# Kernel tuning notes

Hardware: AMD Instinct MI355X
Metric: run time of the kernel (lower is better)

## Reference

```python
import jax, jax.numpy as jnp
import numpy as np

N_NODES = 50000
N_EDGES = 1600000
IN_DIM = 256
HID = 128
HEADS = 1
N_CLASSES = 40
NEG_SLOPE = 0.2


def gat_conv(x, W, a_src, a_dst, b, src, dst, concat):
    """PyG GATConv (eval mode). x: [N, F_in]; W: [H*C, F_in]; a_*: [H, C]; b: bias."""
    N = x.shape[0]
    H, C = a_src.shape
    h = (x @ W.T).reshape(N, H, C)                       # [N, H, C]
    alpha_src = jnp.sum(h * a_src, axis=-1)              # [N, H]
    alpha_dst = jnp.sum(h * a_dst, axis=-1)              # [N, H]
    e = jax.nn.leaky_relu(alpha_src[src] + alpha_dst[dst], NEG_SLOPE)  # [E, H]
    # scatter-softmax over incoming edges of each destination node
    m = jax.ops.segment_max(e, dst, num_segments=N)
    m = jnp.where(jnp.isfinite(m), m, 0.0)               # nodes with no in-edges
    ex = jnp.exp(e - m[dst])
    denom = jax.ops.segment_sum(ex, dst, num_segments=N)
    alpha = ex / jnp.maximum(denom[dst], 1e-16)          # [E, H]
    out = jax.ops.segment_sum(h[src] * alpha[..., None], dst, num_segments=N)  # [N, H, C]
    out = out.reshape(N, H * C) if concat else out.mean(axis=1)
    return out + b


def setup_inputs() -> dict:
    key = jax.random.key(0)
    ks = jax.random.split(key, 10)
    glorot = lambda k, shape: jax.random.normal(k, shape, jnp.float32) * np.sqrt(2.0 / (shape[0] + shape[-1]))
    x = jax.random.normal(ks[0], (N_NODES, IN_DIM), jnp.float32)
    edge_index = jax.random.randint(ks[1], (2, N_EDGES), 0, N_NODES, jnp.int64)
    # layer 0: in=IN_DIM -> hidden, heads=HEADS, concat=True
    W0 = glorot(ks[2], (HEADS * HID, IN_DIM))
    a_src0 = glorot(ks[3], (HEADS, HID))
    a_dst0 = glorot(ks[4], (HEADS, HID))
    b0 = jnp.zeros((HEADS * HID,), jnp.float32)
    # layer 1: in=hidden*heads -> n_classes, concat=False
    W1 = glorot(ks[5], (HEADS * N_CLASSES, HEADS * HID))
    a_src1 = glorot(ks[6], (HEADS, N_CLASSES))
    a_dst1 = glorot(ks[7], (HEADS, N_CLASSES))
    b1 = jnp.zeros((N_CLASSES,), jnp.float32)
    return {"x": x, "edge_index": edge_index,
            "W0": W0, "a_src0": a_src0, "a_dst0": a_dst0, "b0": b0,
            "W1": W1, "a_src1": a_src1, "a_dst1": a_dst1, "b1": b1}


def reference(x, edge_index, W0, a_src0, a_dst0, b0, W1, a_src1, a_dst1, b1):
    N = x.shape[0]
    # PyG GATConv default add_self_loops=True (each layer adds them transiently)
    loop = jnp.arange(N, dtype=edge_index.dtype)
    src = jnp.concatenate([edge_index[0], loop])
    dst = jnp.concatenate([edge_index[1], loop])
    h = gat_conv(x, W0, a_src0, a_dst0, b0, src, dst, concat=True)
    h = jax.nn.relu(h)  # dropout is identity in eval mode
    out = gat_conv(h, W1, a_src1, a_dst1, b1, src, dst, concat=False)
    return out
```

## Files before the change

kernel.cpp:

```cpp
#include <hip/hip_runtime.h>
#include <hip/hip_bf16.h>

#define N_NODES 50000
#define N_EDGES 1600000
#define ET (N_EDGES + N_NODES)
#define IN_DIM 256
#define HID 128
#define NCLS 40
#define NEG 0.2f
#define NBUCK 391
#define CHUNK 4096

typedef short bf16x8 __attribute__((ext_vector_type(8)));
typedef float f32x4  __attribute__((ext_vector_type(4)));

__device__ __forceinline__ unsigned pk2(float a, float b) {
    __hip_bfloat16 ha = __float2bfloat16(a), hb = __float2bfloat16(b);
    unsigned short ua = *(unsigned short*)&ha, ub = *(unsigned short*)&hb;
    return (unsigned)ua | ((unsigned)ub << 16);
}
__device__ __forceinline__ float blo(unsigned u) { return __uint_as_float(u << 16); }
__device__ __forceinline__ float bhi(unsigned u) { return __uint_as_float(u & 0xffff0000u); }

__global__ __launch_bounds__(256) void k_bin_count(const int* __restrict__ ei,
                                                   int* __restrict__ bcnt) {
    __shared__ int hist[NBUCK];
    int t = threadIdx.x;
    for (int i = t; i < NBUCK; i += 256) hist[i] = 0;
    __syncthreads();
    int base = blockIdx.x * CHUNK;
    #pragma unroll
    for (int j = 0; j < 16; ++j) {
        int i = base + j * 256 + t;
        if (i < ET) {
            int d = (i < N_EDGES) ? ei[N_EDGES + i] : (i - N_EDGES);
            atomicAdd(&hist[d >> 7], 1);
        }
    }
    __syncthreads();
    for (int i = t; i < NBUCK; i += 256) if (hist[i]) atomicAdd(&bcnt[i], hist[i]);
}

__global__ __launch_bounds__(512) void k_bin_scan(const int* __restrict__ bcnt,
                                                  int* __restrict__ cstart,
                                                  int* __restrict__ cursor,
                                                  int* __restrict__ rp) {
    __shared__ int s[512];
    int t = threadIdx.x;
    int v = (t < NBUCK) ? bcnt[t] : 0;
    s[t] = v;
    __syncthreads();
    for (int off = 1; off < 512; off <<= 1) {
        int u = (t >= off) ? s[t - off] : 0;
        __syncthreads();
        s[t] += u;
        __syncthreads();
    }
    int ex = s[t] - v;
    if (t < NBUCK) { cstart[t] = ex; cursor[t] = ex; }
    if (t == 0) { cstart[NBUCK] = ET; rp[N_NODES] = ET; }
}

__global__ __launch_bounds__(256) void k_bin_scatter(const int* __restrict__ ei,
                                                     int* __restrict__ cursor,
                                                     unsigned int* __restrict__ buf) {
    __shared__ int sd[CHUNK];
    __shared__ int hist[NBUCK];
    __shared__ int wbase[NBUCK];
    int t = threadIdx.x;
    for (int i = t; i < NBUCK; i += 256) hist[i] = 0;
    __syncthreads();
    int base = blockIdx.x * CHUNK;
    #pragma unroll
    for (int j = 0; j < 16; ++j) {
        int i = base + j * 256 + t;
        int d = -1;
        if (i < ET) d = (i < N_EDGES) ? ei[N_EDGES + i] : (i - N_EDGES);
        sd[j * 256 + t] = d;
        if (d >= 0) atomicAdd(&hist[d >> 7], 1);
    }
    __syncthreads();
    for (int i = t; i < NBUCK; i += 256) {
        int h = hist[i];
        wbase[i] = h ? atomicAdd(&cursor[i], h) : 0;
        hist[i] = 0;
    }
    __syncthreads();
    #pragma unroll
    for (int j = 0; j < 16; ++j) {
        int i = base + j * 256 + t;
        int d = sd[j * 256 + t];
        if (d >= 0) {
            int s_ = (i < N_EDGES) ? ei[i] : d;
            int b = d >> 7;
            int off = atomicAdd(&hist[b], 1);
            buf[wbase[b] + off] = ((unsigned)(d & 127) << 16) | (unsigned)s_;
        }
    }
}

__global__ __launch_bounds__(256) void k_bucket_build(const unsigned int* __restrict__ buf,
                                                      const int* __restrict__ cstart,
                                                      int* __restrict__ rp,
                                                      int* __restrict__ csr) {
    __shared__ int cnt[128], rpl[128], cur[128];
    int b = blockIdx.x;
    int t = threadIdx.x;
    int lo = cstart[b], hi = cstart[b + 1];
    if (t < 128) cnt[t] = 0;
    __syncthreads();
    for (int i = lo + t; i < hi; i += 256) atomicAdd(&cnt[buf[i] >> 16], 1);
    __syncthreads();
    if (t == 0) {
        int run = 0;
        #pragma unroll
        for (int l = 0; l < 128; ++l) { rpl[l] = run; run += cnt[l]; }
    }
    __syncthreads();
    if (t < 128) {
        int node = b * 128 + t;
        if (node < N_NODES) rp[node] = lo + rpl[t];
        cur[t] = 0;
    }
    __syncthreads();
    for (int i = lo + t; i < hi; i += 256) {
        unsigned v = buf[i];
        int dl = v >> 16;
        int off = atomicAdd(&cur[dl], 1);
        csr[lo + rpl[dl] + off] = (int)(v & 0xffffu);
    }
}

__global__ __launch_bounds__(256) void k_gemm0(
    const float* __restrict__ x, const float* __restrict__ W0,
    const float* __restrict__ a_s, const float* __restrict__ a_d,
    unsigned short* __restrict__ h0b, float* __restrict__ as0, float* __restrict__ ad0) {
    __shared__ unsigned sA[64 * 36];
    __shared__ unsigned sB[128 * 36];
    int t = threadIdx.x;
    int n0 = blockIdx.x * 64;
    int w = t >> 6, lane = t & 63;
    int rw = lane & 15, q = lane >> 4;
    f32x4 acc[8];
    #pragma unroll
    for (int n = 0; n < 8; ++n) acc[n] = (f32x4){0.f, 0.f, 0.f, 0.f};

    for (int kc = 0; kc < IN_DIM; kc += 64) {
        #pragma unroll
        for (int i = 0; i < 4; ++i) {
            int f = i * 256 + t;
            int r = f >> 4, fq = f & 15;
            float4 v = make_float4(0.f, 0.f, 0.f, 0.f);
            if (n0 + r < N_NODES)
                v = *(const float4*)&x[(size_t)(n0 + r) * IN_DIM + kc + fq * 4];
            *(uint2*)&sA[r * 36 + fq * 2] = make_uint2(pk2(v.x, v.y), pk2(v.z, v.w));
        }
        #pragma unroll
        for (int i = 0; i < 8; ++i) {
            int f = i * 256 + t;
            int c = f >> 4, fq = f & 15;
            float4 v = *(const float4*)&W0[(size_t)c * IN_DIM + kc + fq * 4];
            *(uint2*)&sB[c * 36 + fq * 2] = make_uint2(pk2(v.x, v.y), pk2(v.z, v.w));
        }
        __syncthreads();
        #pragma unroll
        for (int ks = 0; ks < 2; ++ks) {
            bf16x8 af = *(const bf16x8*)((const unsigned short*)sA + (16 * w + rw) * 72 + ks * 32 + q * 8);
            #pragma unroll
            for (int n = 0; n < 8; ++n) {
                bf16x8 bfr = *(const bf16x8*)((const unsigned short*)sB + (n * 16 + rw) * 72 + ks * 32 + q * 8);
                acc[n] = __builtin_amdgcn_mfma_f32_16x16x32_bf16(af, bfr, acc[n], 0, 0, 0);
            }
        }
        __syncthreads();
    }

    float asv[8], adv[8];
    #pragma unroll
    for (int n = 0; n < 8; ++n) { asv[n] = a_s[n * 16 + rw]; adv[n] = a_d[n * 16 + rw]; }
    float ps[4] = {0.f, 0.f, 0.f, 0.f}, pd[4] = {0.f, 0.f, 0.f, 0.f};
    #pragma unroll
    for (int n = 0; n < 8; ++n)
        #pragma unroll
        for (int reg = 0; reg < 4; ++reg) {
            float vv = acc[n][reg];
            ps[reg] += vv * asv[n];
            pd[reg] += vv * adv[n];
        }
    #pragma unroll
    for (int reg = 0; reg < 4; ++reg) {
        int node = n0 + 16 * w + q * 4 + reg;
        if (node < N_NODES) {
            #pragma unroll
            for (int n = 0; n < 8; ++n) {
                __hip_bfloat16 hb = __float2bfloat16(acc[n][reg]);
                h0b[(size_t)node * HID + n * 16 + rw] = *(unsigned short*)&hb;
            }
        }
    }
    #pragma unroll
    for (int reg = 0; reg < 4; ++reg)
        #pragma unroll
        for (int off = 1; off < 16; off <<= 1) {
            ps[reg] += __shfl_xor(ps[reg], off);
            pd[reg] += __shfl_xor(pd[reg], off);
        }
    if (rw == 0) {
        #pragma unroll
        for (int reg = 0; reg < 4; ++reg) {
            int node = n0 + 16 * w + q * 4 + reg;
            if (node < N_NODES) { as0[node] = ps[reg]; ad0[node] = pd[reg]; }
        }
    }
}

__global__ __launch_bounds__(256) void k_agg0(
    const uint2* __restrict__ h0u, const float* __restrict__ as, const float* __restrict__ ad,
    const int* __restrict__ rp, const int* __restrict__ csr,
    const float* __restrict__ bias, float* __restrict__ act) {
    __shared__ float sw_[4][64];
    __shared__ int   ss_[4][64];
    int wid = threadIdx.x >> 6, lane = threadIdx.x & 63;
    int half = lane >> 5, sl = lane & 31;
    int node = blockIdx.x * 4 + wid;
    int start = rp[node], end = rp[node + 1];
    float ad_n = ad[node];
    float a0 = 0.f, a1 = 0.f, a2 = 0.f, a3 = 0.f, den = 0.f;
    for (int base = start; base < end; base += 64) {
        int mm = end - base; if (mm > 64) mm = 64;
        int s_l = 0; float w_l = 0.f;
        if (lane < mm) {
            s_l = csr[base + lane];
            float e = as[s_l] + ad_n;
            e = (e > 0.f) ? e : NEG * e;
            w_l = __expf(e);
            den += w_l;
        }
        ss_[wid][lane] = s_l;
        sw_[wid][lane] = w_l;
        for (int jj = 0; jj < mm; jj += 8) {
            int i0 = jj + half, i1 = i0 + 2, i2 = i0 + 4, i3 = i0 + 6;
            int   s0 = ss_[wid][i0], s1 = ss_[wid][i1], s2 = ss_[wid][i2], s3 = ss_[wid][i3];
            float w0 = sw_[wid][i0], w1 = sw_[wid][i1], w2 = sw_[wid][i2], w3 = sw_[wid][i3];
            uint2 u0 = h0u[(size_t)s0 * 32 + sl];
            uint2 u1 = h0u[(size_t)s1 * 32 + sl];
            uint2 u2 = h0u[(size_t)s2 * 32 + sl];
            uint2 u3 = h0u[(size_t)s3 * 32 + sl];
            a0 += w0 * blo(u0.x) + w1 * blo(u1.x) + w2 * blo(u2.x) + w3 * blo(u3.x);
            a1 += w0 * bhi(u0.x) + w1 * bhi(u1.x) + w2 * bhi(u2.x) + w3 * bhi(u3.x);
            a2 += w0 * blo(u0.y) + w1 * blo(u1.y) + w2 * blo(u2.y) + w3 * blo(u3.y);
            a3 += w0 * bhi(u0.y) + w1 * bhi(u1.y) + w2 * bhi(u2.y) + w3 * bhi(u3.y);
        }
    }
    #pragma unroll
    for (int off = 32; off; off >>= 1) den += __shfl_xor(den, off);
    a0 += __shfl_xor(a0, 32);
    a1 += __shfl_xor(a1, 32);
    a2 += __shfl_xor(a2, 32);
    a3 += __shfl_xor(a3, 32);
    if (half == 0) {
        float inv = 1.f / fmaxf(den, 1e-16f);
        float4 b4 = *(const float4*)&bias[sl * 4];
        float4 r;
        r.x = fmaxf(a0 * inv + b4.x, 0.f);
        r.y = fmaxf(a1 * inv + b4.y, 0.f);
        r.z = fmaxf(a2 * inv + b4.z, 0.f);
        r.w = fmaxf(a3 * inv + b4.w, 0.f);
        *(float4*)&act[(size_t)node * HID + sl * 4] = r;
    }
}

__global__ __launch_bounds__(128) void k_gemm1(
    const float* __restrict__ act, const float* __restrict__ W1,
    const float* __restrict__ a_s, const float* __restrict__ a_d,
    unsigned short* __restrict__ h1b, float* __restrict__ as1, float* __restrict__ ad1) {
    __shared__ float w1l[NCLS * HID];
    __shared__ float av[NCLS], adv[NCLS];
    int t = threadIdx.x;
    #pragma unroll
    for (int i = 0; i < 10; ++i) {
        int j = t + 128 * i;
        ((float4*)w1l)[j] = ((const float4*)W1)[j];
    }
    if (t < NCLS) { av[t] = a_s[t]; adv[t] = a_d[t]; }
    __syncthreads();
    int n = blockIdx.x * 128 + t;
    if (n >= N_NODES) return;
    const float4* ar = (const float4*)(act + (size_t)n * HID);
    float acc[NCLS];
    #pragma unroll
    for (int c = 0; c < NCLS; ++c) acc[c] = 0.f;
    for (int k0 = 0; k0 < HID; k0 += 4) {
        float4 xv = ar[k0 >> 2];
        #pragma unroll
        for (int c = 0; c < NCLS; ++c) {
            const float4 wv = *(const float4*)&w1l[c * HID + k0];
            acc[c] += xv.x * wv.x + xv.y * wv.y + xv.z * wv.z + xv.w * wv.w;
        }
    }
    float ps = 0.f, pd = 0.f;
    #pragma unroll
    for (int c = 0; c < NCLS; ++c) { ps += acc[c] * av[c]; pd += acc[c] * adv[c]; }
    unsigned pk_[20];
    #pragma unroll
    for (int c = 0; c < 20; ++c) pk_[c] = pk2(acc[2 * c], acc[2 * c + 1]);
    #pragma unroll
    for (int i = 0; i < 5; ++i)
        *(uint4*)&h1b[(size_t)n * NCLS + i * 8] = make_uint4(pk_[4*i], pk_[4*i+1], pk_[4*i+2], pk_[4*i+3]);
    as1[n] = ps; ad1[n] = pd;
}

__global__ __launch_bounds__(256) void k_agg1(
    const unsigned int* __restrict__ h1u, const float* __restrict__ as, const float* __restrict__ ad,
    const int* __restrict__ rp, const int* __restrict__ csr,
    const float* __restrict__ bias, float* __restrict__ out) {
    __shared__ float sw_[4][64];
    __shared__ int   ss_[4][64];
    int wid = threadIdx.x >> 6, lane = threadIdx.x & 63;
    int half = lane >> 5, sl = lane & 31;
    int off20 = (sl < 20) ? sl : 0;
    int node = blockIdx.x * 4 + wid;
    int start = rp[node], end = rp[node + 1];
    float ad_n = ad[node];
    float a0 = 0.f, a1 = 0.f, den = 0.f;
    for (int base = start; base < end; base += 64) {
        int mm = end - base; if (mm > 64) mm = 64;
        int s_l = 0; float w_l = 0.f;
        if (lane < mm) {
            s_l = csr[base + lane];
            float e = as[s_l] + ad_n;
            e = (e > 0.f) ? e : NEG * e;
            w_l = __expf(e);
            den += w_l;
        }
        ss_[wid][lane] = s_l;
        sw_[wid][lane] = w_l;
        for (int jj = 0; jj < mm; jj += 8) {
            int i0 = jj + half, i1 = i0 + 2, i2 = i0 + 4, i3 = i0 + 6;
            int   s0 = ss_[wid][i0], s1 = ss_[wid][i1], s2 = ss_[wid][i2], s3 = ss_[wid][i3];
            float w0 = sw_[wid][i0], w1 = sw_[wid][i1], w2 = sw_[wid][i2], w3 = sw_[wid][i3];
            unsigned u0 = h1u[(size_t)s0 * 20 + off20];
            unsigned u1 = h1u[(size_t)s1 * 20 + off20];
            unsigned u2 = h1u[(size_t)s2 * 20 + off20];
            unsigned u3 = h1u[(size_t)s3 * 20 + off20];
            a0 += w0 * blo(u0) + w1 * blo(u1) + w2 * blo(u2) + w3 * blo(u3);
            a1 += w0 * bhi(u0) + w1 * bhi(u1) + w2 * bhi(u2) + w3 * bhi(u3);
        }
    }
    #pragma unroll
    for (int off = 32; off; off >>= 1) den += __shfl_xor(den, off);
    a0 += __shfl_xor(a0, 32);
    a1 += __shfl_xor(a1, 32);
    if (half == 0 && sl < 20) {
        float inv = 1.f / fmaxf(den, 1e-16f);
        float2 r;
        r.x = a0 * inv + bias[sl * 2];
        r.y = a1 * inv + bias[sl * 2 + 1];
        *(float2*)&out[(size_t)node * NCLS + sl * 2] = r;
    }
}

extern "C" void kernel_launch(void* const* d_in, const int* in_sizes, int n_in,
                              void* d_out, int out_size, void* d_ws, size_t ws_size,
                              hipStream_t stream) {
    const float* x    = (const float*)d_in[0];
    const int*   ei   = (const int*)d_in[1];
    const float* W0   = (const float*)d_in[2];
    const float* a_s0 = (const float*)d_in[3];
    const float* a_d0 = (const float*)d_in[4];
    const float* b0   = (const float*)d_in[5];
    const float* W1   = (const float*)d_in[6];
    const float* a_s1 = (const float*)d_in[7];
    const float* a_d1 = (const float*)d_in[8];
    const float* b1   = (const float*)d_in[9];

    char* p = (char*)d_ws;
    auto alloc = [&](size_t bytes) { void* q = p; p += (bytes + 255) & ~size_t(255); return q; };
    unsigned short* h0b = (unsigned short*)alloc((size_t)N_NODES * HID * 2);
    unsigned short* h1b = (unsigned short*)alloc(((size_t)N_NODES * NCLS + 32) * 2);
    float* act    = (float*)alloc((size_t)N_NODES * HID * 4);
    float* as0    = (float*)alloc((size_t)N_NODES * 4);
    float* ad0    = (float*)alloc((size_t)N_NODES * 4);
    float* as1    = (float*)alloc((size_t)N_NODES * 4);
    float* ad1    = (float*)alloc((size_t)N_NODES * 4);
    int*   rp     = (int*)alloc((size_t)(N_NODES + 1) * 4);
    int*   csr    = (int*)alloc((size_t)ET * 4);
    unsigned int* buf = (unsigned int*)alloc((size_t)ET * 4);
    int*   bcnt   = (int*)alloc((size_t)NBUCK * 4);
    int*   cstart = (int*)alloc((size_t)(NBUCK + 1) * 4);
    int*   cursor = (int*)alloc((size_t)NBUCK * 4);

    const int binWGs = (ET + CHUNK - 1) / CHUNK;
    hipMemsetAsync(bcnt, 0, (size_t)NBUCK * 4, stream);
    k_bin_count<<<binWGs, 256, 0, stream>>>(ei, bcnt);
    k_bin_scan<<<1, 512, 0, stream>>>(bcnt, cstart, cursor, rp);
    k_bin_scatter<<<binWGs, 256, 0, stream>>>(ei, cursor, buf);
    k_bucket_build<<<NBUCK, 256, 0, stream>>>(buf, cstart, rp, csr);
    k_gemm0<<<(N_NODES + 63) / 64, 256, 0, stream>>>(x, W0, a_s0, a_d0, h0b, as0, ad0);
    k_agg0<<<N_NODES / 4, 256, 0, stream>>>((const uint2*)h0b, as0, ad0, rp, csr, b0, act);
    k_gemm1<<<(N_NODES + 127) / 128, 128, 0, stream>>>(act, W1, a_s1, a_d1, h1b, as1, ad1);
    k_agg1<<<N_NODES / 4, 256, 0, stream>>>((const unsigned int*)h1b, as1, ad1, rp, csr, b1, (float*)d_out);
}
```

Measured before the change: 302.6 us.

## Precompute normalized edge weights and shard layer-0 aggregation across feature slices

Adds a separate kernel that computes the softmax edge weights, already normalized, once per layer and stores them per edge. Layer-0 aggregation is split into four feature shards per node, each launched as its own block, with four edge groups of 16 lanes instead of two of 32. The aim is more parallelism and smaller gathers per block. Layer-1 features are written twice into two replicas, and blocks alternate between them to spread gather traffic. The bin buffer now aliases the h0 storage. The costs are extra launches, an edge-sized weight array written and read back, and each CSR row being re-read by four blocks.

```diff
diff --git a/kernel.cpp b/kernel.cpp
--- a/kernel.cpp
+++ b/kernel.cpp
@@ -10,6 +10,7 @@
 #define NEG 0.2f
 #define NBUCK 391
 #define CHUNK 4096
+#define R1D (N_NODES * 20 + 16)
 
 typedef short bf16x8 __attribute__((ext_vector_type(8)));
 typedef float f32x4  __attribute__((ext_vector_type(4)));
@@ -131,6 +132,35 @@
     }
 }
 
+__global__ __launch_bounds__(256) void k_wts(
+    const float* __restrict__ as, const float* __restrict__ ad,
+    const int* __restrict__ rp, const int* __restrict__ csr,
+    float* __restrict__ wn) {
+    int wid = threadIdx.x >> 6, lane = threadIdx.x & 63;
+    int node = blockIdx.x * 4 + wid;
+    int start = rp[node], end = rp[node + 1];
+    float ad_n = ad[node];
+    float den = 0.f;
+    for (int base = start; base < end; base += 64) {
+        int mm = end - base; if (mm > 64) mm = 64;
+        if (lane < mm) {
+            int s = csr[base + lane];
+            float e = as[s] + ad_n;
+            e = (e > 0.f) ? e : NEG * e;
+            float w = __expf(e);
+            den += w;
+            wn[base + lane] = w;
+        }
+    }
+    #pragma unroll
+    for (int off = 32; off; off >>= 1) den += __shfl_xor(den, off);
+    float inv = 1.f / fmaxf(den, 1e-16f);
+    for (int base = start; base < end; base += 64) {
+        int mm = end - base; if (mm > 64) mm = 64;
+        if (lane < mm) wn[base + lane] *= inv;
+    }
+}
+
 __global__ __launch_bounds__(256) void k_gemm0(
     const float* __restrict__ x, const float* __restrict__ W0,
     const float* __restrict__ a_s, const float* __restrict__ a_d,
@@ -215,65 +245,54 @@
 }
 
 __global__ __launch_bounds__(256) void k_agg0(
-    const uint2* __restrict__ h0u, const float* __restrict__ as, const float* __restrict__ ad,
+    const unsigned int* __restrict__ h0d, const float* __restrict__ wn,
     const int* __restrict__ rp, const int* __restrict__ csr,
     const float* __restrict__ bias, float* __restrict__ act) {
     __shared__ float sw_[4][64];
     __shared__ int   ss_[4][64];
     int wid = threadIdx.x >> 6, lane = threadIdx.x & 63;
-    int half = lane >> 5, sl = lane & 31;
-    int node = blockIdx.x * 4 + wid;
+    int shard = blockIdx.x & 3;
+    int node = (blockIdx.x >> 2) * 4 + wid;
+    int q = lane >> 4, ql = lane & 15;
     int start = rp[node], end = rp[node + 1];
-    float ad_n = ad[node];
-    float a0 = 0.f, a1 = 0.f, a2 = 0.f, a3 = 0.f, den = 0.f;
+    const unsigned int* hp = h0d + shard * 16 + ql;
+    float a0 = 0.f, a1 = 0.f;
     for (int base = start; base < end; base += 64) {
         int mm = end - base; if (mm > 64) mm = 64;
         int s_l = 0; float w_l = 0.f;
         if (lane < mm) {
             s_l = csr[base + lane];
-            float e = as[s_l] + ad_n;
-            e = (e > 0.f) ? e : NEG * e;
-            w_l = __expf(e);
-            den += w_l;
+            w_l = wn[base + lane];
         }
         ss_[wid][lane] = s_l;
         sw_[wid][lane] = w_l;
-        for (int jj = 0; jj < mm; jj += 8) {
-            int i0 = jj + half, i1 = i0 + 2, i2 = i0 + 4, i3 = i0 + 6;
+        for (int jj = 0; jj < mm; jj += 16) {
+            int i0 = jj + q, i1 = i0 + 4, i2 = i0 + 8, i3 = i0 + 12;
             int   s0 = ss_[wid][i0], s1 = ss_[wid][i1], s2 = ss_[wid][i2], s3 = ss_[wid][i3];
             float w0 = sw_[wid][i0], w1 = sw_[wid][i1], w2 = sw_[wid][i2], w3 = sw_[wid][i3];
-            uint2 u0 = h0u[(size_t)s0 * 32 + sl];
-            uint2 u1 = h0u[(size_t)s1 * 32 + sl];
-            uint2 u2 = h0u[(size_t)s2 * 32 + sl];
-            uint2 u3 = h0u[(size_t)s3 * 32 + sl];
-            a0 += w0 * blo(u0.x) + w1 * blo(u1.x) + w2 * blo(u2.x) + w3 * blo(u3.x);
-            a1 += w0 * bhi(u0.x) + w1 * bhi(u1.x) + w2 * bhi(u2.x) + w3 * bhi(u3.x);
-            a2 += w0 * blo(u0.y) + w1 * blo(u1.y) + w2 * blo(u2.y) + w3 * blo(u3.y);
-            a3 += w0 * bhi(u0.y) + w1 * bhi(u1.y) + w2 * bhi(u2.y) + w3 * bhi(u3.y);
-        }
-    }
-    #pragma unroll
-    for (int off = 32; off; off >>= 1) den += __shfl_xor(den, off);
-    a0 += __shfl_xor(a0, 32);
-    a1 += __shfl_xor(a1, 32);
-    a2 += __shfl_xor(a2, 32);
-    a3 += __shfl_xor(a3, 32);
-    if (half == 0) {
-        float inv = 1.f / fmaxf(den, 1e-16f);
-        float4 b4 = *(const float4*)&bias[sl * 4];
-        float4 r;
-        r.x = fmaxf(a0 * inv + b4.x, 0.f);
-        r.y = fmaxf(a1 * inv + b4.y, 0.f);
-        r.z = fmaxf(a2 * inv + b4.z, 0.f);
-        r.w = fmaxf(a3 * inv + b4.w, 0.f);
-        *(float4*)&act[(size_t)node * HID + sl * 4] = r;
+            unsigned u0 = hp[(size_t)s0 * 64];
+            unsigned u1 = hp[(size_t)s1 * 64];
+            unsigned u2 = hp[(size_t)s2 * 64];
+            unsigned u3 = hp[(size_t)s3 * 64];
+            a0 += w0 * blo(u0) + w1 * blo(u1) + w2 * blo(u2) + w3 * blo(u3);
+            a1 += w0 * bhi(u0) + w1 * bhi(u1) + w2 * bhi(u2) + w3 * bhi(u3);
+        }
+    }
+    a0 += __shfl_xor(a0, 16); a0 += __shfl_xor(a0, 32);
+    a1 += __shfl_xor(a1, 16); a1 += __shfl_xor(a1, 32);
+    if (lane < 16) {
+        float2 b2 = *(const float2*)&bias[shard * 32 + ql * 2];
+        float2 r;
+        r.x = fmaxf(a0 + b2.x, 0.f);
+        r.y = fmaxf(a1 + b2.y, 0.f);
+        *(float2*)&act[(size_t)node * HID + shard * 32 + ql * 2] = r;
     }
 }
 
 __global__ __launch_bounds__(128) void k_gemm1(
     const float* __restrict__ act, const float* __restrict__ W1,
     const float* __restrict__ a_s, const float* __restrict__ a_d,
-    unsigned short* __restrict__ h1b, float* __restrict__ as1, float* __restrict__ ad1) {
+    unsigned int* __restrict__ h1d, float* __restrict__ as1, float* __restrict__ ad1) {
     __shared__ float w1l[NCLS * HID];
     __shared__ float av[NCLS], adv[NCLS];
     int t = threadIdx.x;
@@ -305,13 +324,16 @@
     #pragma unroll
     for (int c = 0; c < 20; ++c) pk_[c] = pk2(acc[2 * c], acc[2 * c + 1]);
     #pragma unroll
-    for (int i = 0; i < 5; ++i)
-        *(uint4*)&h1b[(size_t)n * NCLS + i * 8] = make_uint4(pk_[4*i], pk_[4*i+1], pk_[4*i+2], pk_[4*i+3]);
+    for (int r = 0; r < 2; ++r)
+        #pragma unroll
+        for (int i = 0; i < 5; ++i)
+            *(uint4*)&h1d[(size_t)r * R1D + (size_t)n * 20 + i * 4] =
+                make_uint4(pk_[4*i], pk_[4*i+1], pk_[4*i+2], pk_[4*i+3]);
     as1[n] = ps; ad1[n] = pd;
 }
 
 __global__ __launch_bounds__(256) void k_agg1(
-    const unsigned int* __restrict__ h1u, const float* __restrict__ as, const float* __restrict__ ad,
+    const unsigned int* __restrict__ h1u, const float* __restrict__ wn,
     const int* __restrict__ rp, const int* __restrict__ csr,
     const float* __restrict__ bias, float* __restrict__ out) {
     __shared__ float sw_[4][64];
@@ -320,18 +342,16 @@
     int half = lane >> 5, sl = lane & 31;
     int off20 = (sl < 20) ? sl : 0;
     int node = blockIdx.x * 4 + wid;
+    int rep = blockIdx.x & 1;
     int start = rp[node], end = rp[node + 1];
-    float ad_n = ad[node];
-    float a0 = 0.f, a1 = 0.f, den = 0.f;
+    const unsigned int* hp = h1u + (size_t)rep * R1D + off20;
+    float a0 = 0.f, a1 = 0.f;
     for (int base = start; base < end; base += 64) {
         int mm = end - base; if (mm > 64) mm = 64;
         int s_l = 0; float w_l = 0.f;
         if (lane < mm) {
             s_l = csr[base + lane];
-            float e = as[s_l] + ad_n;
-            e = (e > 0.f) ? e : NEG * e;
-            w_l = __expf(e);
-            den += w_l;
+            w_l = wn[base + lane];
         }
         ss_[wid][lane] = s_l;
         sw_[wid][lane] = w_l;
@@ -339,23 +359,20 @@
             int i0 = jj + half, i1 = i0 + 2, i2 = i0 + 4, i3 = i0 + 6;
             int   s0 = ss_[wid][i0], s1 = ss_[wid][i1], s2 = ss_[wid][i2], s3 = ss_[wid][i3];
             float w0 = sw_[wid][i0], w1 = sw_[wid][i1], w2 = sw_[wid][i2], w3 = sw_[wid][i3];
-            unsigned u0 = h1u[(size_t)s0 * 20 + off20];
-            unsigned u1 = h1u[(size_t)s1 * 20 + off20];
-            unsigned u2 = h1u[(size_t)s2 * 20 + off20];
-            unsigned u3 = h1u[(size_t)s3 * 20 + off20];
+            unsigned u0 = hp[(size_t)s0 * 20];
+            unsigned u1 = hp[(size_t)s1 * 20];
+            unsigned u2 = hp[(size_t)s2 * 20];
+            unsigned u3 = hp[(size_t)s3 * 20];
             a0 += w0 * blo(u0) + w1 * blo(u1) + w2 * blo(u2) + w3 * blo(u3);
             a1 += w0 * bhi(u0) + w1 * bhi(u1) + w2 * bhi(u2) + w3 * bhi(u3);
         }
     }
-    #pragma unroll
-    for (int off = 32; off; off >>= 1) den += __shfl_xor(den, off);
     a0 += __shfl_xor(a0, 32);
     a1 += __shfl_xor(a1, 32);
     if (half == 0 && sl < 20) {
-        float inv = 1.f / fmaxf(den, 1e-16f);
         float2 r;
-        r.x = a0 * inv + bias[sl * 2];
-        r.y = a1 * inv + bias[sl * 2 + 1];
+        r.x = a0 + bias[sl * 2];
+        r.y = a1 + bias[sl * 2 + 1];
         *(float2*)&out[(size_t)node * NCLS + sl * 2] = r;
     }
 }
@@ -377,7 +394,8 @@
     char* p = (char*)d_ws;
     auto alloc = [&](size_t bytes) { void* q = p; p += (bytes + 255) & ~size_t(255); return q; };
     unsigned short* h0b = (unsigned short*)alloc((size_t)N_NODES * HID * 2);
-    unsigned short* h1b = (unsigned short*)alloc(((size_t)N_NODES * NCLS + 32) * 2);
+    unsigned int*   buf = (unsigned int*)h0b;
+    unsigned int*   h1d = (unsigned int*)alloc((size_t)2 * R1D * 4);
     float* act    = (float*)alloc((size_t)N_NODES * HID * 4);
     float* as0    = (float*)alloc((size_t)N_NODES * 4);
     float* ad0    = (float*)alloc((size_t)N_NODES * 4);
@@ -385,7 +403,7 @@
     float* ad1    = (float*)alloc((size_t)N_NODES * 4);
     int*   rp     = (int*)alloc((size_t)(N_NODES + 1) * 4);
     int*   csr    = (int*)alloc((size_t)ET * 4);
-    unsigned int* buf = (unsigned int*)alloc((size_t)ET * 4);
+    float* wn     = (float*)alloc((size_t)ET * 4);
     int*   bcnt   = (int*)alloc((size_t)NBUCK * 4);
     int*   cstart = (int*)alloc((size_t)(NBUCK + 1) * 4);
     int*   cursor = (int*)alloc((size_t)NBUCK * 4);
@@ -397,7 +415,9 @@
     k_bin_scatter<<<binWGs, 256, 0, stream>>>(ei, cursor, buf);
     k_bucket_build<<<NBUCK, 256, 0, stream>>>(buf, cstart, rp, csr);
     k_gemm0<<<(N_NODES + 63) / 64, 256, 0, stream>>>(x, W0, a_s0, a_d0, h0b, as0, ad0);
-    k_agg0<<<N_NODES / 4, 256, 0, stream>>>((const uint2*)h0b, as0, ad0, rp, csr, b0, act);
-    k_gemm1<<<(N_NODES + 127) / 128, 128, 0, stream>>>(act, W1, a_s1, a_d1, h1b, as1, ad1);
-    k_agg1<<<N_NODES / 4, 256, 0, stream>>>((const unsigned int*)h1b, as1, ad1, rp, csr, b1, (float*)d_out);
-}
+    k_wts<<<N_NODES / 4, 256, 0, stream>>>(as0, ad0, rp, csr, wn);
+    k_agg0<<<N_NODES, 256, 0, stream>>>((const unsigned int*)h0b, wn, rp, csr, b0, act);
+    k_gemm1<<<(N_NODES + 127) / 128, 128, 0, stream>>>(act, W1, a_s1, a_d1, h1d, as1, ad1);
+    k_wts<<<N_NODES / 4, 256, 0, stream>>>(as1, ad1, rp, csr, wn);
+    k_agg1<<<N_NODES / 4, 256, 0, stream>>>(h1d, wn, rp, csr, b1, (float*)d_out);
+}
```

Result: slower. 357.1 us (+18.0%).
